# Optimization experiments

Measured on AMD Instinct MI355X. Metric: run time of the kernel, lower is better.

## Reference

```python
import jax, jax.numpy as jnp
import numpy as np

N_NODES = 100000
N_EDGES = 1600000
HID = 128


def setup_inputs() -> dict:
    key = jax.random.key(0)
    k1, k2, k3, k4, k5 = jax.random.split(key, 5)
    node_embeddings = jax.random.normal(k1, (N_NODES, HID), dtype=jnp.float32)
    src_idx = jax.random.randint(k2, (N_EDGES,), 0, N_NODES, dtype=jnp.int64)
    tgt_idx = jax.random.randint(k3, (N_EDGES,), 0, N_NODES, dtype=jnp.int64)
    # Params of the selected edge-type predictor (Linear(2h,h) -> ReLU -> Linear(h,1))
    W1 = jax.random.normal(k4, (2 * HID, HID), dtype=jnp.float32) * (1.0 / np.sqrt(2 * HID))
    b1 = jnp.zeros((HID,), dtype=jnp.float32)
    W2 = jax.random.normal(k5, (HID, 1), dtype=jnp.float32) * (1.0 / np.sqrt(HID))
    b2 = jnp.zeros((1,), dtype=jnp.float32)
    return {
        "node_embeddings": node_embeddings,
        "src_idx": src_idx,
        "tgt_idx": tgt_idx,
        "edge_type_idx": 0,
        "W1": W1,
        "b1": b1,
        "W2": W2,
        "b2": b2,
    }


def reference(node_embeddings, src_idx, tgt_idx, edge_type_idx, W1, b1, W2, b2):
    # edge_type_idx selects a predictor; params passed in are that predictor's.
    src_emb = node_embeddings[src_idx]  # [E, H]
    tgt_emb = node_embeddings[tgt_idx]  # [E, H]
    # cat([src,tgt]) @ W1 == src @ W1[:H] + tgt @ W1[H:]  (avoids materializing pair_feat)
    h = jax.nn.relu(src_emb @ W1[:HID] + tgt_emb @ W1[HID:] + b1)  # [E, H]
    out = h @ W2 + b2  # [E, 1]
    return out[:, 0]  # squeeze(-1) -> [E]
```

## Files before the change

### kernel.cpp

```cpp
#include <hip/hip_runtime.h>
#include <hip/hip_bf16.h>

#define HID 128

typedef __attribute__((ext_vector_type(8))) short short8;
typedef __attribute__((ext_vector_type(4))) float f32x4;
typedef __attribute__((ext_vector_type(4))) unsigned int u32x4;

__device__ __forceinline__ short f2bf(float x) {
    __bf16 b = (__bf16)x;
    return __builtin_bit_cast(short, b);
}

__global__ void pack_w1_kernel(const float* __restrict__ W1, short* __restrict__ bpk) {
    int t = blockIdx.x * 256 + threadIdx.x;
    int f = (t >> 6) & 7;
    int l = t & 63;
    int n = t >> 9;
    int c = l & 15, kb = l >> 4;
    int k0 = f * 32 + kb * 8;
    short8 v;
#pragma unroll
    for (int j = 0; j < 8; ++j)
        v[j] = f2bf(W1[(k0 + j) * HID + n * 16 + c]);
    *reinterpret_cast<short8*>(&bpk[t * 8]) = v;
}

__global__ __launch_bounds__(256) void conv_emb_kernel(
    const float* __restrict__ emb, short* __restrict__ bemb, int n8) {
    int i = blockIdx.x * 256 + threadIdx.x;
    if (i >= n8) return;
    f32x4 x0 = *reinterpret_cast<const f32x4*>(emb + (size_t)i * 8);
    f32x4 x1 = *reinterpret_cast<const f32x4*>(emb + (size_t)i * 8 + 4);
    short8 v;
#pragma unroll
    for (int j = 0; j < 4; ++j) {
        v[j]     = f2bf(x0[j]);
        v[4 + j] = f2bf(x1[j]);
    }
    *reinterpret_cast<short8*>(&bemb[(size_t)i * 8]) = v;
}

template <int MODE>
__global__ __launch_bounds__(512, 4) void edge_head_kernel(
    const float* __restrict__ emb,
    const short* __restrict__ bemb,
    const void* __restrict__ src_raw,
    const void* __restrict__ tgt_raw,
    const float* __restrict__ W1,
    const float* __restrict__ b1,
    const float* __restrict__ W2,
    const float* __restrict__ b2,
    const short* __restrict__ bpk,
    float* __restrict__ out,
    int E)
{
    __shared__ short lds_b[32768];

    const int tid = threadIdx.x;

    int i64f = 1;
    {
        const int* s32 = (const int*)src_raw;
#pragma unroll
        for (int i = 1; i < 32; i += 2) i64f &= (s32[i] == 0);
    }

    if (MODE != 2) {
        const u32x4* g = (const u32x4*)bpk;
        u32x4* d = (u32x4*)lds_b;
#pragma unroll
        for (int i = 0; i < 8; ++i) d[i * 512 + tid] = g[i * 512 + tid];
    } else {
        for (int i = 0; i < 64; ++i) {
            int idx = i * 512 + tid;
            int col = idx & 127;
            int k   = idx >> 7;
            int n = col >> 4, cc = col & 15;
            int f = k >> 5, kb = (k >> 3) & 3, j = k & 7;
            int l2 = kb * 16 + cc;
            lds_b[(((n * 8 + f) * 64 + l2) << 3) + j] = f2bf(W1[idx]);
        }
    }
    __syncthreads();

    const int l = tid & 63;
    const int wid = tid >> 6;
    const int c = l & 15;
    const int g = l >> 4;
    const long long e0 = (long long)blockIdx.x * 256 + wid * 32;

    unsigned so[2], to[2];
#pragma unroll
    for (int m = 0; m < 2; ++m) {
        long long e = e0 + m * 16 + c;
        if (e >= E) e = E - 1;
        long long si, ti;
        if (i64f) {
            si = ((const long long*)src_raw)[e];
            ti = ((const long long*)tgt_raw)[e];
        } else {
            si = ((const int*)src_raw)[e];
            ti = ((const int*)tgt_raw)[e];
        }
        so[m] = (unsigned)si * HID;
        to[m] = (unsigned)ti * HID;
    }

    f32x4 acc[2][8];
#pragma unroll
    for (int m = 0; m < 2; ++m)
#pragma unroll
        for (int n = 0; n < 8; ++n)
            acc[m][n] = (f32x4){0.f, 0.f, 0.f, 0.f};

    const int koff = g * 8;
#pragma unroll
    for (int f = 0; f < 8; ++f) {
        short8 afr[2];
        const int k0 = (f & 3) * 32 + koff;
#pragma unroll
        for (int m = 0; m < 2; ++m) {
            const unsigned off = (f < 4 ? so[m] : to[m]) + k0;
            if (MODE == 0) {
                afr[m] = *reinterpret_cast<const short8*>(bemb + off);
            } else {
                f32x4 x0 = *reinterpret_cast<const f32x4*>(emb + off);
                f32x4 x1 = *reinterpret_cast<const f32x4*>(emb + off + 4);
                short8 a;
#pragma unroll
                for (int j = 0; j < 4; ++j) {
                    a[j]     = f2bf(x0[j]);
                    a[4 + j] = f2bf(x1[j]);
                }
                afr[m] = a;
            }
        }
#pragma unroll
        for (int n = 0; n < 8; ++n) {
            short8 bfr = *reinterpret_cast<const short8*>(&lds_b[((n * 8 + f) * 64 + l) * 8]);
#pragma unroll
            for (int m = 0; m < 2; ++m)
                acc[m][n] = __builtin_amdgcn_mfma_f32_16x16x32_bf16(afr[m], bfr, acc[m][n], 0, 0, 0);
        }
    }

    float b1v[8], w2v[8];
#pragma unroll
    for (int n = 0; n < 8; ++n) {
        b1v[n] = b1[n * 16 + c];
        w2v[n] = W2[n * 16 + c];
    }
    const float b2s = b2[0];

#pragma unroll
    for (int m = 0; m < 2; ++m) {
        float s[4] = {0.f, 0.f, 0.f, 0.f};
#pragma unroll
        for (int n = 0; n < 8; ++n) {
#pragma unroll
            for (int r = 0; r < 4; ++r)
                s[r] += fmaxf(acc[m][n][r] + b1v[n], 0.f) * w2v[n];
        }
#pragma unroll
        for (int w = 1; w < 16; w <<= 1) {
#pragma unroll
            for (int r = 0; r < 4; ++r)
                s[r] += __shfl_xor(s[r], w, 16);
        }
        if (c == 0) {
            const long long eb = e0 + m * 16 + g * 4;
#pragma unroll
            for (int r = 0; r < 4; ++r)
                if (eb + r < E) out[eb + r] = s[r] + b2s;
        }
    }
}

extern "C" void kernel_launch(void* const* d_in, const int* in_sizes, int n_in,
                              void* d_out, int out_size, void* d_ws, size_t ws_size,
                              hipStream_t stream) {
    const float* emb = (const float*)d_in[0];
    const void*  src = d_in[1];
    const void*  tgt = d_in[2];
    const float* W1 = (const float*)d_in[4];
    const float* b1 = (const float*)d_in[5];
    const float* W2 = (const float*)d_in[6];
    const float* b2 = (const float*)d_in[7];
    float* out = (float*)d_out;

    const int E = in_sizes[1];
    const int embN = in_sizes[0];
    const size_t need_full = 65536 + (size_t)embN * sizeof(short);

    short* bpk  = (short*)d_ws;
    short* bemb = (short*)((char*)d_ws + 65536);

    int mode;
    if (ws_size >= need_full)       mode = 0;
    else if (ws_size >= 65536)      mode = 1;
    else                            mode = 2;

    if (mode != 2)
        pack_w1_kernel<<<16, 256, 0, stream>>>(W1, bpk);
    if (mode == 0) {
        const int n8 = embN / 8;
        conv_emb_kernel<<<(n8 + 255) / 256, 256, 0, stream>>>(emb, bemb, n8);
    }

    const int grid = (E + 255) / 256;
    if (mode == 0)
        edge_head_kernel<0><<<grid, 512, 0, stream>>>(emb, bemb, src, tgt, W1, b1, W2, b2, bpk, out, E);
    else if (mode == 1)
        edge_head_kernel<1><<<grid, 512, 0, stream>>>(emb, bemb, src, tgt, W1, b1, W2, b2, bpk, out, E);
    else
        edge_head_kernel<2><<<grid, 512, 0, stream>>>(emb, bemb, src, tgt, W1, b1, W2, b2, bpk, out, E);
}
```

Baseline: 160.3 us.

## Retile edge head as 2x2 wave grid and prefetch gathers before W1 staging

Blocks shrink to 256 threads covering 128 edges, with waves laid out as two edge halves times two hidden-column halves. Each wave now computes a 64x64 tile, so each B fragment read from LDS feeds four MFMAs instead of two. Partial output sums from the two column halves are combined through a small LDS buffer. In the bf16 path, all A-fragment gathers are issued before the W1 copy into LDS and the barrier, so gather latency overlaps that staging. The cost is that every block stages the full 64 KB W1 copy for half as many edges, plus higher register use from holding 32 A fragments per thread.

```diff
diff --git a/kernel.cpp b/kernel.cpp
--- a/kernel.cpp
+++ b/kernel.cpp
@@ -42,7 +42,7 @@
 }
 
 template <int MODE>
-__global__ __launch_bounds__(512, 4) void edge_head_kernel(
+__global__ __launch_bounds__(256, 2) void edge_head_kernel(
     const float* __restrict__ emb,
     const short* __restrict__ bemb,
     const void* __restrict__ src_raw,
@@ -56,8 +56,15 @@
     int E)
 {
     __shared__ short lds_b[32768];
+    __shared__ float lds_part[128];
 
     const int tid = threadIdx.x;
+    const int l = tid & 63;
+    const int wid = tid >> 6;
+    const int we = wid & 1;
+    const int wn = wid >> 1;
+    const int c = l & 15;
+    const int g = l >> 4;
 
     int i64f = 1;
     {
@@ -66,33 +73,11 @@
         for (int i = 1; i < 32; i += 2) i64f &= (s32[i] == 0);
     }
 
-    if (MODE != 2) {
-        const u32x4* g = (const u32x4*)bpk;
-        u32x4* d = (u32x4*)lds_b;
-#pragma unroll
-        for (int i = 0; i < 8; ++i) d[i * 512 + tid] = g[i * 512 + tid];
-    } else {
-        for (int i = 0; i < 64; ++i) {
-            int idx = i * 512 + tid;
-            int col = idx & 127;
-            int k   = idx >> 7;
-            int n = col >> 4, cc = col & 15;
-            int f = k >> 5, kb = (k >> 3) & 3, j = k & 7;
-            int l2 = kb * 16 + cc;
-            lds_b[(((n * 8 + f) * 64 + l2) << 3) + j] = f2bf(W1[idx]);
-        }
-    }
-    __syncthreads();
-
-    const int l = tid & 63;
-    const int wid = tid >> 6;
-    const int c = l & 15;
-    const int g = l >> 4;
-    const long long e0 = (long long)blockIdx.x * 256 + wid * 32;
-
-    unsigned so[2], to[2];
-#pragma unroll
-    for (int m = 0; m < 2; ++m) {
+    const long long e0 = (long long)blockIdx.x * 128 + we * 64;
+
+    unsigned so[4], to[4];
+#pragma unroll
+    for (int m = 0; m < 4; ++m) {
         long long e = e0 + m * 16 + c;
         if (e >= E) e = E - 1;
         long long si, ti;
@@ -107,57 +92,100 @@
         to[m] = (unsigned)ti * HID;
     }
 
-    f32x4 acc[2][8];
-#pragma unroll
-    for (int m = 0; m < 2; ++m)
-#pragma unroll
-        for (int n = 0; n < 8; ++n)
+    if (MODE != 2) {
+        const u32x4* gsrc = (const u32x4*)bpk;
+        u32x4* d = (u32x4*)lds_b;
+#pragma unroll
+        for (int i = 0; i < 16; ++i) d[i * 256 + tid] = gsrc[i * 256 + tid];
+    } else {
+        for (int i = 0; i < 128; ++i) {
+            int idx = i * 256 + tid;
+            int col = idx & 127;
+            int k   = idx >> 7;
+            int n = col >> 4, cc = col & 15;
+            int f = k >> 5, kb = (k >> 3) & 3, j = k & 7;
+            int l2 = kb * 16 + cc;
+            lds_b[(((n * 8 + f) * 64 + l2) << 3) + j] = f2bf(W1[idx]);
+        }
+    }
+
+    f32x4 acc[4][4];
+#pragma unroll
+    for (int m = 0; m < 4; ++m)
+#pragma unroll
+        for (int n = 0; n < 4; ++n)
             acc[m][n] = (f32x4){0.f, 0.f, 0.f, 0.f};
 
     const int koff = g * 8;
-#pragma unroll
-    for (int f = 0; f < 8; ++f) {
-        short8 afr[2];
-        const int k0 = (f & 3) * 32 + koff;
-#pragma unroll
-        for (int m = 0; m < 2; ++m) {
-            const unsigned off = (f < 4 ? so[m] : to[m]) + k0;
-            if (MODE == 0) {
-                afr[m] = *reinterpret_cast<const short8*>(bemb + off);
-            } else {
+
+    if (MODE == 0) {
+        short8 a[8][4];
+#pragma unroll
+        for (int f = 0; f < 8; ++f) {
+            const int k0 = (f & 3) * 32 + koff;
+#pragma unroll
+            for (int m = 0; m < 4; ++m) {
+                const unsigned off = (f < 4 ? so[m] : to[m]) + k0;
+                a[f][m] = *reinterpret_cast<const short8*>(bemb + off);
+            }
+        }
+        __syncthreads();
+#pragma unroll
+        for (int f = 0; f < 8; ++f) {
+#pragma unroll
+            for (int n = 0; n < 4; ++n) {
+                const int nt = wn * 4 + n;
+                short8 bfr = *reinterpret_cast<const short8*>(&lds_b[((nt * 8 + f) * 64 + l) * 8]);
+#pragma unroll
+                for (int m = 0; m < 4; ++m)
+                    acc[m][n] = __builtin_amdgcn_mfma_f32_16x16x32_bf16(a[f][m], bfr, acc[m][n], 0, 0, 0);
+            }
+        }
+    } else {
+        __syncthreads();
+#pragma unroll
+        for (int f = 0; f < 8; ++f) {
+            const int k0 = (f & 3) * 32 + koff;
+            short8 afr[4];
+#pragma unroll
+            for (int m = 0; m < 4; ++m) {
+                const unsigned off = (f < 4 ? so[m] : to[m]) + k0;
                 f32x4 x0 = *reinterpret_cast<const f32x4*>(emb + off);
                 f32x4 x1 = *reinterpret_cast<const f32x4*>(emb + off + 4);
-                short8 a;
+                short8 t;
 #pragma unroll
                 for (int j = 0; j < 4; ++j) {
-                    a[j]     = f2bf(x0[j]);
-                    a[4 + j] = f2bf(x1[j]);
+                    t[j]     = f2bf(x0[j]);
+                    t[4 + j] = f2bf(x1[j]);
                 }
-                afr[m] = a;
-            }
-        }
-#pragma unroll
-        for (int n = 0; n < 8; ++n) {
-            short8 bfr = *reinterpret_cast<const short8*>(&lds_b[((n * 8 + f) * 64 + l) * 8]);
-#pragma unroll
-            for (int m = 0; m < 2; ++m)
-                acc[m][n] = __builtin_amdgcn_mfma_f32_16x16x32_bf16(afr[m], bfr, acc[m][n], 0, 0, 0);
-        }
-    }
-
-    float b1v[8], w2v[8];
-#pragma unroll
-    for (int n = 0; n < 8; ++n) {
-        b1v[n] = b1[n * 16 + c];
-        w2v[n] = W2[n * 16 + c];
+                afr[m] = t;
+            }
+#pragma unroll
+            for (int n = 0; n < 4; ++n) {
+                const int nt = wn * 4 + n;
+                short8 bfr = *reinterpret_cast<const short8*>(&lds_b[((nt * 8 + f) * 64 + l) * 8]);
+#pragma unroll
+                for (int m = 0; m < 4; ++m)
+                    acc[m][n] = __builtin_amdgcn_mfma_f32_16x16x32_bf16(afr[m], bfr, acc[m][n], 0, 0, 0);
+            }
+        }
+    }
+
+    float b1v[4], w2v[4];
+#pragma unroll
+    for (int n = 0; n < 4; ++n) {
+        const int col = wn * 64 + n * 16 + c;
+        b1v[n] = b1[col];
+        w2v[n] = W2[col];
     }
     const float b2s = b2[0];
 
-#pragma unroll
-    for (int m = 0; m < 2; ++m) {
+    float sm[4][4];
+#pragma unroll
+    for (int m = 0; m < 4; ++m) {
         float s[4] = {0.f, 0.f, 0.f, 0.f};
 #pragma unroll
-        for (int n = 0; n < 8; ++n) {
+        for (int n = 0; n < 4; ++n) {
 #pragma unroll
             for (int r = 0; r < 4; ++r)
                 s[r] += fmaxf(acc[m][n][r] + b1v[n], 0.f) * w2v[n];
@@ -168,12 +196,27 @@
             for (int r = 0; r < 4; ++r)
                 s[r] += __shfl_xor(s[r], w, 16);
         }
-        if (c == 0) {
-            const long long eb = e0 + m * 16 + g * 4;
+#pragma unroll
+        for (int r = 0; r < 4; ++r) sm[m][r] = s[r];
+    }
+
+    if (wn == 0 && c == 0) {
+#pragma unroll
+        for (int m = 0; m < 4; ++m)
 #pragma unroll
             for (int r = 0; r < 4; ++r)
-                if (eb + r < E) out[eb + r] = s[r] + b2s;
-        }
+                lds_part[we * 64 + m * 16 + g * 4 + r] = sm[m][r];
+    }
+    __syncthreads();
+    if (wn == 1 && c == 0) {
+#pragma unroll
+        for (int m = 0; m < 4; ++m)
+#pragma unroll
+            for (int r = 0; r < 4; ++r) {
+                const long long e = e0 + m * 16 + g * 4 + r;
+                if (e < E)
+                    out[e] = sm[m][r] + lds_part[we * 64 + m * 16 + g * 4 + r] + b2s;
+            }
     }
 }
 
@@ -208,11 +251,11 @@
         conv_emb_kernel<<<(n8 + 255) / 256, 256, 0, stream>>>(emb, bemb, n8);
     }
 
-    const int grid = (E + 255) / 256;
+    const int grid = (E + 127) / 128;
     if (mode == 0)
-        edge_head_kernel<0><<<grid, 512, 0, stream>>>(emb, bemb, src, tgt, W1, b1, W2, b2, bpk, out, E);
+        edge_head_kernel<0><<<grid, 256, 0, stream>>>(emb, bemb, src, tgt, W1, b1, W2, b2, bpk, out, E);
     else if (mode == 1)
-        edge_head_kernel<1><<<grid, 512, 0, stream>>>(emb, bemb, src, tgt, W1, b1, W2, b2, bpk, out, E);
+        edge_head_kernel<1><<<grid, 256, 0, stream>>>(emb, bemb, src, tgt, W1, b1, W2, b2, bpk, out, E);
     else
-        edge_head_kernel<2><<<grid, 512, 0, stream>>>(emb, bemb, src, tgt, W1, b1, W2, b2, bpk, out, E);
-}
+        edge_head_kernel<2><<<grid, 256, 0, stream>>>(emb, bemb, src, tgt, W1, b1, W2, b2, bpk, out, E);
+}
```

Result: slower. 260.5 us (median of 5 runs) (+62.5%).

## Switch to 32x32x16 MFMA tiles with N-split waves and register double-buffered gathers

Applied to the files above, without the earlier changes.

Moves the per-edge MLP from 16x16x32 MFMAs to 32x32x16 bf16 MFMAs. Each pair of waves now covers 64 edges, and each wave of the pair handles half of the 128 hidden columns, so W1 is repacked into a matching LDS layout. Gathered embedding fragments are double-buffered in registers so the next k-step's loads are in flight during the current MFMAs, and the index loads are issued before the LDS weight fill. The two column halves are reduced through LDS with an extra block barrier, which adds longer shuffle-reduction chains and more accumulator registers.

```diff
diff --git a/kernel.cpp b/kernel.cpp
--- a/kernel.cpp
+++ b/kernel.cpp
@@ -5,6 +5,7 @@
 
 typedef __attribute__((ext_vector_type(8))) short short8;
 typedef __attribute__((ext_vector_type(4))) float f32x4;
+typedef __attribute__((ext_vector_type(16))) float f32x16;
 typedef __attribute__((ext_vector_type(4))) unsigned int u32x4;
 
 __device__ __forceinline__ short f2bf(float x) {
@@ -14,15 +15,15 @@
 
 __global__ void pack_w1_kernel(const float* __restrict__ W1, short* __restrict__ bpk) {
     int t = blockIdx.x * 256 + threadIdx.x;
-    int f = (t >> 6) & 7;
-    int l = t & 63;
-    int n = t >> 9;
-    int c = l & 15, kb = l >> 4;
-    int k0 = f * 32 + kb * 8;
+    int l  = t & 63;
+    int ks = (t >> 6) & 15;
+    int nt = t >> 10;
+    int k0  = ks * 16 + (l >> 5) * 8;
+    int col = nt * 32 + (l & 31);
     short8 v;
 #pragma unroll
     for (int j = 0; j < 8; ++j)
-        v[j] = f2bf(W1[(k0 + j) * HID + n * 16 + c]);
+        v[j] = f2bf(W1[(k0 + j) * HID + col]);
     *reinterpret_cast<short8*>(&bpk[t * 8]) = v;
 }
 
@@ -56,8 +57,15 @@
     int E)
 {
     __shared__ short lds_b[32768];
+    __shared__ float lds_part[256];
 
     const int tid = threadIdx.x;
+    const int l   = tid & 63;
+    const int wid = tid >> 6;
+    const int we  = wid >> 1;
+    const int wn  = wid & 1;
+    const int lc  = l & 31;
+    const int hi  = l >> 5;
 
     int i64f = 1;
     {
@@ -66,34 +74,12 @@
         for (int i = 1; i < 32; i += 2) i64f &= (s32[i] == 0);
     }
 
-    if (MODE != 2) {
-        const u32x4* g = (const u32x4*)bpk;
-        u32x4* d = (u32x4*)lds_b;
-#pragma unroll
-        for (int i = 0; i < 8; ++i) d[i * 512 + tid] = g[i * 512 + tid];
-    } else {
-        for (int i = 0; i < 64; ++i) {
-            int idx = i * 512 + tid;
-            int col = idx & 127;
-            int k   = idx >> 7;
-            int n = col >> 4, cc = col & 15;
-            int f = k >> 5, kb = (k >> 3) & 3, j = k & 7;
-            int l2 = kb * 16 + cc;
-            lds_b[(((n * 8 + f) * 64 + l2) << 3) + j] = f2bf(W1[idx]);
-        }
-    }
-    __syncthreads();
-
-    const int l = tid & 63;
-    const int wid = tid >> 6;
-    const int c = l & 15;
-    const int g = l >> 4;
-    const long long e0 = (long long)blockIdx.x * 256 + wid * 32;
+    const long long e0 = (long long)blockIdx.x * 256 + we * 64;
 
     unsigned so[2], to[2];
 #pragma unroll
     for (int m = 0; m < 2; ++m) {
-        long long e = e0 + m * 16 + c;
+        long long e = e0 + m * 32 + lc;
         if (e >= E) e = E - 1;
         long long si, ti;
         if (i64f) {
@@ -107,73 +93,128 @@
         to[m] = (unsigned)ti * HID;
     }
 
-    f32x4 acc[2][8];
+    if (MODE != 2) {
+        const u32x4* gsrc = (const u32x4*)bpk;
+        u32x4* d = (u32x4*)lds_b;
+#pragma unroll
+        for (int i = 0; i < 8; ++i) d[i * 512 + tid] = gsrc[i * 512 + tid];
+    } else {
+        for (int i = 0; i < 64; ++i) {
+            int idx = i * 512 + tid;
+            int k   = idx >> 7;
+            int col = idx & 127;
+            int nt = col >> 5, lcc = col & 31;
+            int ks = k >> 4,  kr = k & 15;
+            int h2 = kr >> 3, j = kr & 7;
+            int l2 = h2 * 32 + lcc;
+            lds_b[(((nt * 16 + ks) * 64 + l2) << 3) + j] = f2bf(W1[idx]);
+        }
+    }
+    __syncthreads();
+
+    f32x16 acc[2][2];
 #pragma unroll
     for (int m = 0; m < 2; ++m)
 #pragma unroll
-        for (int n = 0; n < 8; ++n)
-            acc[m][n] = (f32x4){0.f, 0.f, 0.f, 0.f};
-
-    const int koff = g * 8;
-#pragma unroll
-    for (int f = 0; f < 8; ++f) {
-        short8 afr[2];
-        const int k0 = (f & 3) * 32 + koff;
-#pragma unroll
-        for (int m = 0; m < 2; ++m) {
-            const unsigned off = (f < 4 ? so[m] : to[m]) + k0;
-            if (MODE == 0) {
-                afr[m] = *reinterpret_cast<const short8*>(bemb + off);
-            } else {
-                f32x4 x0 = *reinterpret_cast<const f32x4*>(emb + off);
-                f32x4 x1 = *reinterpret_cast<const f32x4*>(emb + off + 4);
-                short8 a;
-#pragma unroll
-                for (int j = 0; j < 4; ++j) {
-                    a[j]     = f2bf(x0[j]);
-                    a[4 + j] = f2bf(x1[j]);
+        for (int n = 0; n < 2; ++n)
+            acc[m][n] = (f32x16)(0.f);
+
+    const unsigned asub = hi * 8;
+
+    short8 abuf[2][2];
+#pragma unroll
+    for (int m = 0; m < 2; ++m) {
+        if (MODE == 0) {
+            abuf[0][m] = *reinterpret_cast<const short8*>(bemb + so[m] + asub);
+        } else {
+            const float* p = emb + so[m] + asub;
+            f32x4 x0 = *reinterpret_cast<const f32x4*>(p);
+            f32x4 x1 = *reinterpret_cast<const f32x4*>(p + 4);
+            short8 t;
+#pragma unroll
+            for (int j = 0; j < 4; ++j) { t[j] = f2bf(x0[j]); t[4 + j] = f2bf(x1[j]); }
+            abuf[0][m] = t;
+        }
+    }
+
+#pragma unroll
+    for (int ks = 0; ks < 16; ++ks) {
+        const int cur = ks & 1, nxt = cur ^ 1;
+        if (ks < 15) {
+            const int ks1 = ks + 1;
+            const unsigned koff = (unsigned)(ks1 & 7) * 16 + asub;
+#pragma unroll
+            for (int m = 0; m < 2; ++m) {
+                const unsigned off = (ks1 < 8 ? so[m] : to[m]) + koff;
+                if (MODE == 0) {
+                    abuf[nxt][m] = *reinterpret_cast<const short8*>(bemb + off);
+                } else {
+                    const float* p = emb + off;
+                    f32x4 x0 = *reinterpret_cast<const f32x4*>(p);
+                    f32x4 x1 = *reinterpret_cast<const f32x4*>(p + 4);
+                    short8 t;
+#pragma unroll
+                    for (int j = 0; j < 4; ++j) { t[j] = f2bf(x0[j]); t[4 + j] = f2bf(x1[j]); }
+                    abuf[nxt][m] = t;
                 }
-                afr[m] = a;
             }
         }
 #pragma unroll
-        for (int n = 0; n < 8; ++n) {
-            short8 bfr = *reinterpret_cast<const short8*>(&lds_b[((n * 8 + f) * 64 + l) * 8]);
+        for (int n = 0; n < 2; ++n) {
+            const int nt = wn * 2 + n;
+            short8 bfr = *reinterpret_cast<const short8*>(&lds_b[((nt * 16 + ks) * 64 + l) * 8]);
 #pragma unroll
             for (int m = 0; m < 2; ++m)
-                acc[m][n] = __builtin_amdgcn_mfma_f32_16x16x32_bf16(afr[m], bfr, acc[m][n], 0, 0, 0);
-        }
-    }
-
-    float b1v[8], w2v[8];
-#pragma unroll
-    for (int n = 0; n < 8; ++n) {
-        b1v[n] = b1[n * 16 + c];
-        w2v[n] = W2[n * 16 + c];
+                acc[m][n] = __builtin_amdgcn_mfma_f32_32x32x16_bf16(abuf[cur][m], bfr, acc[m][n], 0, 0, 0);
+        }
+    }
+
+    float b1v[2], w2v[2];
+#pragma unroll
+    for (int n = 0; n < 2; ++n) {
+        const int col = wn * 64 + n * 32 + lc;
+        b1v[n] = b1[col];
+        w2v[n] = W2[col];
     }
     const float b2s = b2[0];
 
+    float sm[2][16];
 #pragma unroll
     for (int m = 0; m < 2; ++m) {
-        float s[4] = {0.f, 0.f, 0.f, 0.f};
-#pragma unroll
-        for (int n = 0; n < 8; ++n) {
-#pragma unroll
-            for (int r = 0; r < 4; ++r)
-                s[r] += fmaxf(acc[m][n][r] + b1v[n], 0.f) * w2v[n];
-        }
-#pragma unroll
-        for (int w = 1; w < 16; w <<= 1) {
-#pragma unroll
-            for (int r = 0; r < 4; ++r)
-                s[r] += __shfl_xor(s[r], w, 16);
-        }
-        if (c == 0) {
-            const long long eb = e0 + m * 16 + g * 4;
-#pragma unroll
-            for (int r = 0; r < 4; ++r)
-                if (eb + r < E) out[eb + r] = s[r] + b2s;
-        }
+#pragma unroll
+        for (int r = 0; r < 16; ++r) {
+            float s = fmaxf(acc[m][0][r] + b1v[0], 0.f) * w2v[0]
+                    + fmaxf(acc[m][1][r] + b1v[1], 0.f) * w2v[1];
+            sm[m][r] = s;
+        }
+#pragma unroll
+        for (int w = 1; w < 32; w <<= 1) {
+#pragma unroll
+            for (int r = 0; r < 16; ++r)
+                sm[m][r] += __shfl_xor(sm[m][r], w, 32);
+        }
+    }
+
+    if (wn == 0 && lc == 0) {
+#pragma unroll
+        for (int m = 0; m < 2; ++m)
+#pragma unroll
+            for (int r = 0; r < 16; ++r) {
+                const int row = m * 32 + (r & 3) + 8 * (r >> 2) + 4 * hi;
+                lds_part[we * 64 + row] = sm[m][r];
+            }
+    }
+    __syncthreads();
+    if (wn == 1 && lc == 0) {
+#pragma unroll
+        for (int m = 0; m < 2; ++m)
+#pragma unroll
+            for (int r = 0; r < 16; ++r) {
+                const int row = m * 32 + (r & 3) + 8 * (r >> 2) + 4 * hi;
+                const long long e = e0 + row;
+                if (e < E)
+                    out[e] = sm[m][r] + lds_part[we * 64 + row] + b2s;
+            }
     }
 }
 
```

Measured after the change: 282.3 us. 76.1% more time.

## Precompute per-node W1 projections, then gather and combine per edge

Applied to the files above, without the earlier changes.

Splits the computation into a per-node GEMM that produces U = emb@W1[:H] and V = emb@W1[H:] in bf16, followed by a lightweight per-edge pass that gathers U[src] and V[tgt], adds b1, applies ReLU and takes the dot product with W2. This removes the per-edge matmul, since there are 16x more edges than nodes, and replaces it with a 100k-row GEMM plus gathers of two bf16 rows per edge. Rounding the intermediate projections to bf16 adds some error, and the path needs workspace large enough to hold both U and V.

```diff
diff --git a/kernel.cpp b/kernel.cpp
--- a/kernel.cpp
+++ b/kernel.cpp
@@ -5,12 +5,174 @@
 
 typedef __attribute__((ext_vector_type(8))) short short8;
 typedef __attribute__((ext_vector_type(4))) float f32x4;
+typedef __attribute__((ext_vector_type(16))) float f32x16;
 typedef __attribute__((ext_vector_type(4))) unsigned int u32x4;
 
 __device__ __forceinline__ short f2bf(float x) {
     __bf16 b = (__bf16)x;
     return __builtin_bit_cast(short, b);
 }
+__device__ __forceinline__ float bf2f(short s) {
+    unsigned u = (unsigned)(unsigned short)s << 16;
+    return __builtin_bit_cast(float, u);
+}
+
+
+__global__ void pack_w1_uv_kernel(const float* __restrict__ W1, short* __restrict__ bpk2) {
+    int t = blockIdx.x * 256 + threadIdx.x;
+    int l    = t & 63;
+    int ks   = (t >> 6) & 7;
+    int nt   = (t >> 9) & 3;
+    int half = t >> 11;
+    int k0  = half * 128 + ks * 16 + (l >> 5) * 8;
+    int col = nt * 32 + (l & 31);
+    short8 v;
+#pragma unroll
+    for (int j = 0; j < 8; ++j)
+        v[j] = f2bf(W1[(k0 + j) * HID + col]);
+    *reinterpret_cast<short8*>(&bpk2[t * 8]) = v;
+}
+
+__global__ __launch_bounds__(512, 4) void uv_kernel(
+    const float* __restrict__ emb,
+    const short* __restrict__ bpk2,
+    short* __restrict__ U,
+    short* __restrict__ V,
+    int Nn)
+{
+    __shared__ short lds_b[32768];
+
+    const int tid = threadIdx.x;
+    const int l   = tid & 63;
+    const int wid = tid >> 6;
+    const int wg  = wid >> 1;
+    const int wn  = wid & 1;
+    const int lc  = l & 31;
+    const int hi  = l >> 5;
+
+    {
+        const u32x4* g = (const u32x4*)bpk2;
+        u32x4* d = (u32x4*)lds_b;
+#pragma unroll
+        for (int i = 0; i < 8; ++i) d[i * 512 + tid] = g[i * 512 + tid];
+    }
+    __syncthreads();
+
+    const int base = blockIdx.x * 128 + wg * 32;
+    int nr = base + lc;
+    if (nr >= Nn) nr = Nn - 1;
+
+    f32x16 accU[2], accV[2];
+#pragma unroll
+    for (int n = 0; n < 2; ++n) { accU[n] = (f32x16)(0.f); accV[n] = (f32x16)(0.f); }
+
+#pragma unroll
+    for (int ks = 0; ks < 8; ++ks) {
+        const float* p = emb + (size_t)nr * HID + ks * 16 + hi * 8;
+        f32x4 x0 = *reinterpret_cast<const f32x4*>(p);
+        f32x4 x1 = *reinterpret_cast<const f32x4*>(p + 4);
+        short8 afr;
+#pragma unroll
+        for (int j = 0; j < 4; ++j) { afr[j] = f2bf(x0[j]); afr[4 + j] = f2bf(x1[j]); }
+#pragma unroll
+        for (int n = 0; n < 2; ++n) {
+            const int nt = wn * 2 + n;
+            short8 bU = *reinterpret_cast<const short8*>(&lds_b[(((0 + nt) * 8 + ks) * 64 + l) * 8]);
+            short8 bV = *reinterpret_cast<const short8*>(&lds_b[(((4 + nt) * 8 + ks) * 64 + l) * 8]);
+            accU[n] = __builtin_amdgcn_mfma_f32_32x32x16_bf16(afr, bU, accU[n], 0, 0, 0);
+            accV[n] = __builtin_amdgcn_mfma_f32_32x32x16_bf16(afr, bV, accV[n], 0, 0, 0);
+        }
+    }
+
+#pragma unroll
+    for (int n = 0; n < 2; ++n) {
+        const int col = wn * 64 + n * 32 + lc;
+#pragma unroll
+        for (int r = 0; r < 16; ++r) {
+            const int row = (r & 3) + 8 * (r >> 2) + 4 * hi;
+            const int node = base + row;
+            if (node < Nn) {
+                U[(size_t)node * HID + col] = f2bf(accU[n][r]);
+                V[(size_t)node * HID + col] = f2bf(accV[n][r]);
+            }
+        }
+    }
+}
+
+__global__ __launch_bounds__(256) void edge_pass_kernel(
+    const short* __restrict__ U,
+    const short* __restrict__ V,
+    const void* __restrict__ src_raw,
+    const void* __restrict__ tgt_raw,
+    const float* __restrict__ b1,
+    const float* __restrict__ W2,
+    const float* __restrict__ b2,
+    float* __restrict__ out,
+    int E)
+{
+    const int tid = threadIdx.x;
+    const int l   = tid & 63;
+    const int wid = tid >> 6;
+    const int le  = l >> 4;
+    const int lc  = l & 15;
+
+    int i64f = 1;
+    {
+        const int* s32 = (const int*)src_raw;
+#pragma unroll
+        for (int i = 1; i < 32; i += 2) i64f &= (s32[i] == 0);
+    }
+
+    float b1v[8], w2v[8];
+    {
+        f32x4 a = *reinterpret_cast<const f32x4*>(b1 + lc * 8);
+        f32x4 b = *reinterpret_cast<const f32x4*>(b1 + lc * 8 + 4);
+        f32x4 c = *reinterpret_cast<const f32x4*>(W2 + lc * 8);
+        f32x4 d = *reinterpret_cast<const f32x4*>(W2 + lc * 8 + 4);
+#pragma unroll
+        for (int j = 0; j < 4; ++j) {
+            b1v[j] = a[j]; b1v[4 + j] = b[j];
+            w2v[j] = c[j]; w2v[4 + j] = d[j];
+        }
+    }
+    const float b2s = b2[0];
+
+    const long long ebase = ((long long)blockIdx.x * 4 + wid) * 16;
+
+    short8 ub[4], vb[4];
+#pragma unroll
+    for (int g = 0; g < 4; ++g) {
+        long long e = ebase + g * 4 + le;
+        if (e >= E) e = E - 1;
+        long long si, ti;
+        if (i64f) {
+            si = ((const long long*)src_raw)[e];
+            ti = ((const long long*)tgt_raw)[e];
+        } else {
+            si = ((const int*)src_raw)[e];
+            ti = ((const int*)tgt_raw)[e];
+        }
+        ub[g] = *reinterpret_cast<const short8*>(U + (unsigned)si * HID + lc * 8);
+        vb[g] = *reinterpret_cast<const short8*>(V + (unsigned)ti * HID + lc * 8);
+    }
+
+#pragma unroll
+    for (int g = 0; g < 4; ++g) {
+        float s = 0.f;
+#pragma unroll
+        for (int j = 0; j < 8; ++j) {
+            float h = bf2f(ub[g][j]) + bf2f(vb[g][j]) + b1v[j];
+            s += fmaxf(h, 0.f) * w2v[j];
+        }
+#pragma unroll
+        for (int w = 1; w < 16; w <<= 1)
+            s += __shfl_xor(s, w, 16);
+        const long long e = ebase + g * 4 + le;
+        if (lc == 0 && e < E)
+            out[e] = s + b2s;
+    }
+}
+
 
 __global__ void pack_w1_kernel(const float* __restrict__ W1, short* __restrict__ bpk) {
     int t = blockIdx.x * 256 + threadIdx.x;
@@ -127,13 +289,13 @@
             } else {
                 f32x4 x0 = *reinterpret_cast<const f32x4*>(emb + off);
                 f32x4 x1 = *reinterpret_cast<const f32x4*>(emb + off + 4);
-                short8 a;
+                short8 t;
 #pragma unroll
                 for (int j = 0; j < 4; ++j) {
-                    a[j]     = f2bf(x0[j]);
-                    a[4 + j] = f2bf(x1[j]);
+                    t[j]     = f2bf(x0[j]);
+                    t[4 + j] = f2bf(x1[j]);
                 }
-                afr[m] = a;
+                afr[m] = t;
             }
         }
 #pragma unroll
@@ -189,22 +351,36 @@
     const float* b2 = (const float*)d_in[7];
     float* out = (float*)d_out;
 
-    const int E = in_sizes[1];
-    const int embN = in_sizes[0];
-    const size_t need_full = 65536 + (size_t)embN * sizeof(short);
+    const int E  = in_sizes[1];
+    const int Nn = in_sizes[0] / HID;
+
+    const size_t uv_bytes   = (size_t)Nn * HID * sizeof(short);
+    const size_t need_uv    = 65536 + 2 * uv_bytes;
+    const size_t need_old   = 65536 + (size_t)in_sizes[0] * sizeof(short);
+
+    if (ws_size >= need_uv) {
+        short* bpk2 = (short*)d_ws;
+        short* U    = (short*)((char*)d_ws + 65536);
+        short* Vv   = (short*)((char*)d_ws + 65536 + uv_bytes);
+
+        pack_w1_uv_kernel<<<16, 256, 0, stream>>>(W1, bpk2);
+        uv_kernel<<<(Nn + 127) / 128, 512, 0, stream>>>(emb, bpk2, U, Vv, Nn);
+        edge_pass_kernel<<<(E + 63) / 64, 256, 0, stream>>>(U, Vv, src, tgt, b1, W2, b2, out, E);
+        return;
+    }
 
     short* bpk  = (short*)d_ws;
     short* bemb = (short*)((char*)d_ws + 65536);
 
     int mode;
-    if (ws_size >= need_full)       mode = 0;
+    if (ws_size >= need_old)        mode = 0;
     else if (ws_size >= 65536)      mode = 1;
     else                            mode = 2;
 
     if (mode != 2)
         pack_w1_kernel<<<16, 256, 0, stream>>>(W1, bpk);
     if (mode == 0) {
-        const int n8 = embN / 8;
+        const int n8 = in_sizes[0] / 8;
         conv_emb_kernel<<<(n8 + 255) / 256, 256, 0, stream>>>(emb, bemb, n8);
     }
 
```

After: 141.9 us. -11.5%, faster.
